# Kernel tuning notes

Hardware: AMD Instinct MI355X
Metric: run time of the kernel (lower is better)

The kernel has to match this reference:

```python
import jax, jax.numpy as jnp
import numpy as np

B, L, D, H, R = 2, 2048, 1024, 16, 32
DH = D // H
LORA_SCALE = 64.0 / 32.0  # alpha / rank


def _ln(x, w, b):
    mu = jnp.mean(x, axis=-1, keepdims=True)
    xc = x - mu
    var = jnp.mean(xc * xc, axis=-1, keepdims=True)
    y = xc * jax.lax.rsqrt(var + 1e-5) * w
    return y + b if b is not None else y


def _rotate_half(x):
    x1, x2 = jnp.split(x, 2, axis=-1)
    return jnp.concatenate([-x2, x1], axis=-1)


def _apply_rotary(q, k):
    # q, k: [B, L, H, DH]
    seqlen = q.shape[1]
    inv_freq = 1.0 / (10000.0 ** (jnp.arange(0, DH, 2, dtype=jnp.float32) / DH))
    t = jnp.arange(seqlen, dtype=jnp.float32)
    freqs = t[:, None] * inv_freq[None, :]           # [L, DH/2]
    emb = jnp.concatenate([freqs, freqs], axis=-1)   # [L, DH]
    cos = jnp.cos(emb)[None, :, None, :]
    sin = jnp.sin(emb)[None, :, None, :]
    q = q * cos + _rotate_half(q) * sin
    k = k * cos + _rotate_half(k) * sin
    return q, k


def setup_inputs() -> dict:
    key = jax.random.key(0)
    ks = jax.random.split(key, 10)
    s = 0.02
    return {
        "x": jax.random.normal(ks[0], (B, L, D), dtype=jnp.float32),
        "seq_id": jnp.sort(jax.random.randint(ks[1], (B, L), 0, 4), axis=-1),
        "ln_w": jnp.ones((D,), jnp.float32),
        "ln_b": jnp.zeros((D,), jnp.float32),
        "w_qkv": jax.random.normal(ks[2], (3 * D, D), jnp.float32) * s,
        "q_lora_a": jax.random.normal(ks[3], (R, D), jnp.float32) * s,
        "q_lora_b": jax.random.normal(ks[4], (D, R), jnp.float32) * s,
        "v_lora_a": jax.random.normal(ks[5], (R, D), jnp.float32) * s,
        "v_lora_b": jax.random.normal(ks[6], (D, R), jnp.float32) * s,
        "q_ln_w": jnp.ones((D,), jnp.float32),
        "k_ln_w": jnp.ones((D,), jnp.float32),
        "w_out": jax.random.normal(ks[7], (D, D), jnp.float32) * s,
    }


def reference(x, seq_id, ln_w, ln_b, w_qkv, q_lora_a, q_lora_b,
              v_lora_a, v_lora_b, q_ln_w, k_ln_w, w_out):
    h = _ln(x, ln_w, ln_b)                          # [B, L, D]
    qkv = jnp.einsum('bld,ed->ble', h, w_qkv)       # [B, L, 3D]
    q, k, v = jnp.split(qkv, 3, axis=-1)
    q = q + LORA_SCALE * jnp.einsum('blr,dr->bld', jnp.einsum('bld,rd->blr', h, q_lora_a), q_lora_b)
    v = v + LORA_SCALE * jnp.einsum('blr,dr->bld', jnp.einsum('bld,rd->blr', h, v_lora_a), v_lora_b)
    q = _ln(q, q_ln_w, None)
    k = _ln(k, k_ln_w, None)
    q = q.reshape(B, L, H, DH)
    k = k.reshape(B, L, H, DH)
    q, k = _apply_rotary(q, k)
    qh = q.transpose(0, 2, 1, 3)                    # [B, H, L, DH]
    kh = k.transpose(0, 2, 1, 3)
    vh = v.reshape(B, L, H, DH).transpose(0, 2, 1, 3)
    scale = 1.0 / np.sqrt(DH)
    scores = jnp.einsum('bhqd,bhkd->bhqk', qh, kh) * scale
    mask = (seq_id[:, None, :, None] == seq_id[:, None, None, :])  # [B,1,L,L]
    scores = jnp.where(mask, scores, jnp.finfo(scores.dtype).min)
    attn = jax.nn.softmax(scores, axis=-1)
    ctx = jnp.einsum('bhqk,bhkd->bhqd', attn, vh)   # [B, H, L, DH]
    ctx = ctx.transpose(0, 2, 1, 3).reshape(B, L, D)
    return jnp.einsum('bld,ed->ble', ctx, w_out)
```

## Files before the change

### kernel.cpp

```cpp
#include <hip/hip_runtime.h>
#include <hip/hip_bf16.h>
#include <cmath>

constexpr int Bb = 2;
constexpr int Ls = 2048;
constexpr int Dd = 1024;
constexpr int Hh = 16;
constexpr int DHh = 64;
constexpr int Rr = 32;
constexpr int BL = Bb * Ls;
constexpr float LORA_SCALE = 2.0f;
constexpr float LN_EPS = 1e-5f;
constexpr float ATTN_SCALE = 0.125f;
constexpr float LOG2E = 1.4426950408889634f;
constexpr float QSCL = ATTN_SCALE * LOG2E;

typedef __attribute__((ext_vector_type(8))) short bf16x8;
typedef __attribute__((ext_vector_type(4))) float f32x4;

__device__ __forceinline__ unsigned short f2bf(float f) {
    __hip_bfloat16 b = __float2bfloat16(f);
    return *reinterpret_cast<unsigned short*>(&b);
}
__device__ __forceinline__ float bf2f(unsigned short u) {
    unsigned int x = ((unsigned int)u) << 16;
    return __uint_as_float(x);
}
__device__ __forceinline__ void async_copy16(const void* g, void* l) {
    __builtin_amdgcn_global_load_lds(
        (__attribute__((address_space(1))) void*)(void*)(size_t)g,
        (__attribute__((address_space(3))) void*)l, 16, 0, 0);
}

__global__ __launch_bounds__(256) void prep_ln_kernel(const float* __restrict__ w,
                                                      const float* __restrict__ qa,
                                                      const float* __restrict__ qb,
                                                      const float* __restrict__ va,
                                                      const float* __restrict__ vb,
                                                      const float* __restrict__ wout,
                                                      const float* __restrict__ x,
                                                      const float* __restrict__ lnw,
                                                      const float* __restrict__ lnb,
                                                      unsigned short* __restrict__ wqkvb,
                                                      unsigned short* __restrict__ woutb,
                                                      float* __restrict__ ropec,
                                                      float* __restrict__ ropes,
                                                      unsigned short* __restrict__ hb) {
    const int blk = blockIdx.x;
    const int tid = threadIdx.x;
    if (blk < 3 * Dd) {
        const int e = blk;
        const int d0 = tid * 4;
        __shared__ float br[Rr];
        const bool isq = (e < Dd);
        const bool isv = (e >= 2 * Dd);
        const float* bsrc = isq ? (qb + (size_t)e * Rr)
                                : (isv ? (vb + (size_t)(e - 2 * Dd) * Rr) : nullptr);
        const float* asrc = isq ? qa : va;
        if (bsrc && tid < Rr) br[tid] = bsrc[tid];
        __syncthreads();
        float acc[4] = {0.f, 0.f, 0.f, 0.f};
        if (bsrc) {
#pragma unroll 8
            for (int r = 0; r < Rr; ++r) {
                float4 av = *(const float4*)(asrc + (size_t)r * Dd + d0);
                acc[0] += br[r] * av.x; acc[1] += br[r] * av.y;
                acc[2] += br[r] * av.z; acc[3] += br[r] * av.w;
            }
        }
        float4 wv = *(const float4*)(w + (size_t)e * Dd + d0);
        ushort4 o;
        o.x = f2bf(wv.x + LORA_SCALE * acc[0]);
        o.y = f2bf(wv.y + LORA_SCALE * acc[1]);
        o.z = f2bf(wv.z + LORA_SCALE * acc[2]);
        o.w = f2bf(wv.w + LORA_SCALE * acc[3]);
        *(ushort4*)(wqkvb + (size_t)e * Dd + d0) = o;
    } else if (blk < 4 * Dd) {
        int i = ((blk - 3 * Dd) * 256 + tid) * 4;
        float4 v = *(const float4*)(wout + i);
        ushort4 o;
        o.x = f2bf(v.x); o.y = f2bf(v.y); o.z = f2bf(v.z); o.w = f2bf(v.w);
        *(ushort4*)(woutb + i) = o;
    } else if (blk < 4 * Dd + 256) {
        int i = (blk - 4 * Dd) * 256 + tid;
        int l = i >> 5;
        int f = i & 31;
        float invf = powf(10000.0f, -(float)f * (1.0f / 32.0f));
        float ang = (float)l * invf;
        float s, c;
        sincosf(ang, &s, &c);
        ropec[i] = c;
        ropes[i] = s;
    } else {
        const int w64 = tid >> 6;
        const int L = tid & 63;
        const int row = (blk - (4 * Dd + 256)) * 4 + w64;
        const float* xr = x + (size_t)row * Dd;
        float4 v4[4];
        float v[16];
#pragma unroll
        for (int c = 0; c < 4; ++c) {
            v4[c] = *(const float4*)(xr + c * 256 + L * 4);
            v[c * 4 + 0] = v4[c].x; v[c * 4 + 1] = v4[c].y;
            v[c * 4 + 2] = v4[c].z; v[c * 4 + 3] = v4[c].w;
        }
        float s = 0.f;
#pragma unroll
        for (int j = 0; j < 16; ++j) s += v[j];
#pragma unroll
        for (int off = 1; off < 64; off <<= 1) s += __shfl_xor(s, off, 64);
        float mean = s * (1.0f / Dd);
        float sq = 0.f;
#pragma unroll
        for (int j = 0; j < 16; ++j) {
            v[j] -= mean;
            sq += v[j] * v[j];
        }
#pragma unroll
        for (int off = 1; off < 64; off <<= 1) sq += __shfl_xor(sq, off, 64);
        float rs = rsqrtf(sq * (1.0f / Dd) + LN_EPS);
        unsigned short* hr = hb + (size_t)row * Dd;
#pragma unroll
        for (int c = 0; c < 4; ++c) {
            int d = c * 256 + L * 4;
            float4 wv = *(const float4*)(lnw + d);
            float4 bv = *(const float4*)(lnb + d);
            ushort4 o;
            o.x = f2bf(v[c * 4 + 0] * rs * wv.x + bv.x);
            o.y = f2bf(v[c * 4 + 1] * rs * wv.y + bv.y);
            o.z = f2bf(v[c * 4 + 2] * rs * wv.z + bv.z);
            o.w = f2bf(v[c * 4 + 3] * rs * wv.w + bv.w);
            *(ushort4*)(hr + d) = o;
        }
    }
}

__global__ __launch_bounds__(256) void gemm_bt_mfma(const unsigned short* __restrict__ A,
                                                    const unsigned short* __restrict__ B,
                                                    unsigned short* __restrict__ C,
                                                    int M, int N, int K) {
    __shared__ short As[128 * 64];
    __shared__ short Bs[128 * 64];
    const int tid = threadIdx.x;
    const int w = tid >> 6, lane = tid & 63, quad = lane >> 4, l15 = lane & 15;
    const int m0 = blockIdx.y * 128, n0 = blockIdx.x * 128;
    const int wm = (w & 1) * 64, wn = (w >> 1) * 64;
    f32x4 acc[4][4];
#pragma unroll
    for (int i = 0; i < 4; ++i)
#pragma unroll
        for (int j = 0; j < 4; ++j) acc[i][j] = f32x4{0.f, 0.f, 0.f, 0.f};

    for (int k0 = 0; k0 < K; k0 += 64) {
#pragma unroll
        for (int j = 0; j < 4; ++j) {
            int c = tid + j * 256;
            int row = c >> 3;
            int jg = (c & 7) ^ (row & 7);
            async_copy16(A + (size_t)(m0 + row) * K + k0 + jg * 8, As + c * 8);
        }
#pragma unroll
        for (int j = 0; j < 4; ++j) {
            int c = tid + j * 256;
            int row = c >> 3;
            int jg = (c & 7) ^ (row & 7);
            async_copy16(B + (size_t)(n0 + row) * K + k0 + jg * 8, Bs + c * 8);
        }
        __syncthreads();
#pragma unroll
        for (int ks = 0; ks < 2; ++ks) {
            bf16x8 a[4], b[4];
#pragma unroll
            for (int mi = 0; mi < 4; ++mi) {
                int row = wm + mi * 16 + l15;
                int ch = (ks * 4 + quad) ^ (row & 7);
                a[mi] = *(const bf16x8*)&As[row * 64 + ch * 8];
            }
#pragma unroll
            for (int ni = 0; ni < 4; ++ni) {
                int row = wn + ni * 16 + l15;
                int ch = (ks * 4 + quad) ^ (row & 7);
                b[ni] = *(const bf16x8*)&Bs[row * 64 + ch * 8];
            }
#pragma unroll
            for (int mi = 0; mi < 4; ++mi)
#pragma unroll
                for (int ni = 0; ni < 4; ++ni)
                    acc[mi][ni] = __builtin_amdgcn_mfma_f32_16x16x32_bf16(a[mi], b[ni], acc[mi][ni], 0, 0, 0);
        }
        __syncthreads();
    }
#pragma unroll
    for (int mi = 0; mi < 4; ++mi)
#pragma unroll
        for (int ni = 0; ni < 4; ++ni)
#pragma unroll
            for (int r = 0; r < 4; ++r)
                C[(size_t)(m0 + wm + mi * 16 + quad * 4 + r) * N + n0 + wn + ni * 16 + l15] =
                    f2bf(acc[mi][ni][r]);
}

__global__ __launch_bounds__(256) void gemm_bt_mfma_n64(const unsigned short* __restrict__ A,
                                                        const unsigned short* __restrict__ B,
                                                        float* __restrict__ C,
                                                        int M, int N, int K) {
    __shared__ short As[128 * 64];
    __shared__ short Bs[64 * 64];
    const int tid = threadIdx.x;
    const int w = tid >> 6, lane = tid & 63, quad = lane >> 4, l15 = lane & 15;
    const int m0 = blockIdx.y * 128, n0 = blockIdx.x * 64;
    const int wm = (w & 1) * 64, wn = (w >> 1) * 32;
    f32x4 acc[4][2];
#pragma unroll
    for (int i = 0; i < 4; ++i)
#pragma unroll
        for (int j = 0; j < 2; ++j) acc[i][j] = f32x4{0.f, 0.f, 0.f, 0.f};

    for (int k0 = 0; k0 < K; k0 += 64) {
#pragma unroll
        for (int j = 0; j < 4; ++j) {
            int c = tid + j * 256;
            int row = c >> 3;
            int jg = (c & 7) ^ (row & 7);
            async_copy16(A + (size_t)(m0 + row) * K + k0 + jg * 8, As + c * 8);
        }
#pragma unroll
        for (int j = 0; j < 2; ++j) {
            int c = tid + j * 256;
            int row = c >> 3;
            int jg = (c & 7) ^ (row & 7);
            async_copy16(B + (size_t)(n0 + row) * K + k0 + jg * 8, Bs + c * 8);
        }
        __syncthreads();
#pragma unroll
        for (int ks = 0; ks < 2; ++ks) {
            bf16x8 a[4], b[2];
#pragma unroll
            for (int mi = 0; mi < 4; ++mi) {
                int row = wm + mi * 16 + l15;
                int ch = (ks * 4 + quad) ^ (row & 7);
                a[mi] = *(const bf16x8*)&As[row * 64 + ch * 8];
            }
#pragma unroll
            for (int ni = 0; ni < 2; ++ni) {
                int row = wn + ni * 16 + l15;
                int ch = (ks * 4 + quad) ^ (row & 7);
                b[ni] = *(const bf16x8*)&Bs[row * 64 + ch * 8];
            }
#pragma unroll
            for (int mi = 0; mi < 4; ++mi)
#pragma unroll
                for (int ni = 0; ni < 2; ++ni)
                    acc[mi][ni] = __builtin_amdgcn_mfma_f32_16x16x32_bf16(a[mi], b[ni], acc[mi][ni], 0, 0, 0);
        }
        __syncthreads();
    }
#pragma unroll
    for (int mi = 0; mi < 4; ++mi)
#pragma unroll
        for (int ni = 0; ni < 2; ++ni)
#pragma unroll
            for (int r = 0; r < 4; ++r)
                C[(size_t)(m0 + wm + mi * 16 + quad * 4 + r) * N + n0 + wn + ni * 16 + l15] =
                    acc[mi][ni][r];
}

__global__ __launch_bounds__(256) void qkv_final_kernel(const unsigned short* __restrict__ qkvb,
                                                        const float* __restrict__ qlnw,
                                                        const float* __restrict__ klnw,
                                                        const float* __restrict__ ropec,
                                                        const float* __restrict__ ropes,
                                                        unsigned short* __restrict__ qt,
                                                        unsigned short* __restrict__ kt,
                                                        unsigned short* __restrict__ vtt) {
    const int blk = blockIdx.x;
    const int tid = threadIdx.x;
    if (blk < BL / 4) {
        const int w64 = tid >> 6;
        const int L = tid & 63;
        const int row = blk * 4 + w64;
        const int b = row >> 11;
        const int l = row & (Ls - 1);
        const unsigned short* qp = qkvb + (size_t)row * (3 * Dd);
        const unsigned short* kp = qp + Dd;

        bf16x8 qA = *(const bf16x8*)(qp + L * 8);
        bf16x8 qB = *(const bf16x8*)(qp + 512 + L * 8);
        bf16x8 kA = *(const bf16x8*)(kp + L * 8);
        bf16x8 kB = *(const bf16x8*)(kp + 512 + L * 8);
        float vq[16], vk[16];
#pragma unroll
        for (int j = 0; j < 8; ++j) {
            vq[j] = bf2f((unsigned short)qA[j]);
            vq[8 + j] = bf2f((unsigned short)qB[j]);
            vk[j] = bf2f((unsigned short)kA[j]);
            vk[8 + j] = bf2f((unsigned short)kB[j]);
        }
        float sq = 0.f, sk = 0.f;
#pragma unroll
        for (int j = 0; j < 16; ++j) { sq += vq[j]; sk += vk[j]; }
#pragma unroll
        for (int off = 1; off < 64; off <<= 1) {
            sq += __shfl_xor(sq, off, 64);
            sk += __shfl_xor(sk, off, 64);
        }
        float mq = sq * (1.0f / Dd), mk = sk * (1.0f / Dd);
        float vvq = 0.f, vvk = 0.f;
#pragma unroll
        for (int j = 0; j < 16; ++j) {
            vq[j] -= mq; vvq += vq[j] * vq[j];
            vk[j] -= mk; vvk += vk[j] * vk[j];
        }
#pragma unroll
        for (int off = 1; off < 64; off <<= 1) {
            vvq += __shfl_xor(vvq, off, 64);
            vvk += __shfl_xor(vvk, off, 64);
        }
        float rsq = rsqrtf(vvq * (1.0f / Dd) + LN_EPS);
        float rsk = rsqrtf(vvk * (1.0f / Dd) + LN_EPS);

        float yq[16], yk[16];
        {
            float4 w0 = *(const float4*)(qlnw + L * 8);
            float4 w1 = *(const float4*)(qlnw + L * 8 + 4);
            float4 w2 = *(const float4*)(qlnw + 512 + L * 8);
            float4 w3 = *(const float4*)(qlnw + 512 + L * 8 + 4);
            yq[0] = vq[0] * rsq * w0.x; yq[1] = vq[1] * rsq * w0.y;
            yq[2] = vq[2] * rsq * w0.z; yq[3] = vq[3] * rsq * w0.w;
            yq[4] = vq[4] * rsq * w1.x; yq[5] = vq[5] * rsq * w1.y;
            yq[6] = vq[6] * rsq * w1.z; yq[7] = vq[7] * rsq * w1.w;
            yq[8] = vq[8] * rsq * w2.x; yq[9] = vq[9] * rsq * w2.y;
            yq[10] = vq[10] * rsq * w2.z; yq[11] = vq[11] * rsq * w2.w;
            yq[12] = vq[12] * rsq * w3.x; yq[13] = vq[13] * rsq * w3.y;
            yq[14] = vq[14] * rsq * w3.z; yq[15] = vq[15] * rsq * w3.w;
        }
        {
            float4 w0 = *(const float4*)(klnw + L * 8);
            float4 w1 = *(const float4*)(klnw + L * 8 + 4);
            float4 w2 = *(const float4*)(klnw + 512 + L * 8);
            float4 w3 = *(const float4*)(klnw + 512 + L * 8 + 4);
            yk[0] = vk[0] * rsk * w0.x; yk[1] = vk[1] * rsk * w0.y;
            yk[2] = vk[2] * rsk * w0.z; yk[3] = vk[3] * rsk * w0.w;
            yk[4] = vk[4] * rsk * w1.x; yk[5] = vk[5] * rsk * w1.y;
            yk[6] = vk[6] * rsk * w1.z; yk[7] = vk[7] * rsk * w1.w;
            yk[8] = vk[8] * rsk * w2.x; yk[9] = vk[9] * rsk * w2.y;
            yk[10] = vk[10] * rsk * w2.z; yk[11] = vk[11] * rsk * w2.w;
            yk[12] = vk[12] * rsk * w3.x; yk[13] = vk[13] * rsk * w3.y;
            yk[14] = vk[14] * rsk * w3.z; yk[15] = vk[15] * rsk * w3.w;
        }

        float cs[8], sn[8];
        {
            int fbase = l * 32 + (L & 3) * 8;
            float4 c0 = *(const float4*)(ropec + fbase);
            float4 c1 = *(const float4*)(ropec + fbase + 4);
            float4 s0 = *(const float4*)(ropes + fbase);
            float4 s1 = *(const float4*)(ropes + fbase + 4);
            cs[0] = c0.x; cs[1] = c0.y; cs[2] = c0.z; cs[3] = c0.w;
            cs[4] = c1.x; cs[5] = c1.y; cs[6] = c1.z; cs[7] = c1.w;
            sn[0] = s0.x; sn[1] = s0.y; sn[2] = s0.z; sn[3] = s0.w;
            sn[4] = s1.x; sn[5] = s1.y; sn[6] = s1.z; sn[7] = s1.w;
        }
        const float sgn = (L & 4) ? 1.0f : -1.0f;
        unsigned short outqA[8], outqB[8], outkA[8], outkB[8];
#pragma unroll
        for (int j = 0; j < 8; ++j) {
            float pA = __shfl_xor(yq[j], 4, 64);
            float pB = __shfl_xor(yq[8 + j], 4, 64);
            outqA[j] = f2bf((yq[j] * cs[j] + sgn * pA * sn[j]) * QSCL);
            outqB[j] = f2bf((yq[8 + j] * cs[j] + sgn * pB * sn[j]) * QSCL);
            float pkA = __shfl_xor(yk[j], 4, 64);
            float pkB = __shfl_xor(yk[8 + j], 4, 64);
            outkA[j] = f2bf(yk[j] * cs[j] + sgn * pkA * sn[j]);
            outkB[j] = f2bf(yk[8 + j] * cs[j] + sgn * pkB * sn[j]);
        }
        const int hA = L >> 3;
        const int dh0 = (L & 7) * 8;
        size_t offA = (((size_t)(b * Hh + hA)) * Ls + l) * DHh + dh0;
        size_t offB = (((size_t)(b * Hh + 8 + hA)) * Ls + l) * DHh + dh0;
        *(uint4*)(qt + offA) = *(uint4*)outqA;
        *(uint4*)(qt + offB) = *(uint4*)outqB;
        *(uint4*)(kt + offA) = *(uint4*)outkA;
        *(uint4*)(kt + offB) = *(uint4*)outkB;
    } else {
        const int t2 = blk - BL / 4;
        const int l0 = (t2 & 31) * 64;
        const int h = (t2 >> 5) & 15;
        const int b = t2 >> 9;
        __shared__ short t[64][72];
        const unsigned short* src = qkvb + (size_t)b * Ls * (3 * Dd) + 2 * Dd + h * 64;
#pragma unroll
        for (int j = 0; j < 2; ++j) {
            int g = tid + j * 256;
            int row = g >> 3;
            int c0 = (g & 7) * 8;
            uint4 vv = *(const uint4*)(src + (size_t)(l0 + row) * (3 * Dd) + c0);
            *(uint4*)&t[row][c0] = vv;
        }
        __syncthreads();
        unsigned short* dst = vtt + ((size_t)(b * Hh + h) * DHh) * Ls;
#pragma unroll
        for (int j = 0; j < 2; ++j) {
            int g = tid + j * 256;
            int dh = g >> 3;
            int lc = (g & 7) * 8;
            ushort4 o0, o1;
            unsigned short* p0 = (unsigned short*)&o0;
            unsigned short* p1 = (unsigned short*)&o1;
#pragma unroll
            for (int i = 0; i < 4; ++i) p0[i] = (unsigned short)t[lc + i][dh];
#pragma unroll
            for (int i = 0; i < 4; ++i) p1[i] = (unsigned short)t[lc + 4 + i][dh];
            *(ushort4*)(dst + (size_t)dh * Ls + l0 + lc) = o0;
            *(ushort4*)(dst + (size_t)dh * Ls + l0 + lc + 4) = o1;
        }
    }
}

constexpr int PSP = 76;

__global__ __launch_bounds__(512) void attn_kernel(const unsigned short* __restrict__ qt,
                                                   const unsigned short* __restrict__ kt,
                                                   const unsigned short* __restrict__ vtt,
                                                   const int* __restrict__ seq_id,
                                                   unsigned short* __restrict__ ctxb) {
    const int id = blockIdx.x;
    const int c8 = id & 7;
    const int x = (id >> 3) & 15;
    const int g4 = id >> 7;
    const int v = c8 + 8 * g4;
    const int b = v >> 4;
    const int h = v & 15;
    const int q0 = x * 128;

    const size_t base = ((size_t)(b * Hh + h)) * Ls * DHh;
    const size_t base_v = ((size_t)(b * Hh + h)) * DHh * Ls;
    const int* sid = seq_id + (size_t)b * Ls;

    __shared__ short Ks[2][64 * 64];
    __shared__ short Vs[2][64 * 64];
    __shared__ short Ps[8][16 * PSP];
    __shared__ int sq_s[128];

    const int tid = threadIdx.x;
    const int w = tid >> 6;
    const int lane = tid & 63;
    const int quad = lane >> 4;
    const int l15 = lane & 15;

    if (tid < 128) sq_s[tid] = sid[q0 + tid];
    const int qmin = sid[q0];
    const int qmax = sid[q0 + 127];

    bool need = false;
    if (lane < 32) {
        int kmn = sid[lane * 64];
        int kmx = sid[lane * 64 + 63];
        need = (kmn <= qmax) && (kmx >= qmin);
    }
    unsigned long long bmask = __ballot(need);
    const int t0 = __builtin_ctzll(bmask);
    const int t1 = 64 - __builtin_clzll(bmask);

    auto stage = [&](int buf, int t) {
        int row = tid >> 3;
        int jg = (tid & 7) ^ (row & 7);
        async_copy16(kt + base + (size_t)(t * 64 + row) * DHh + jg * 8,
                     &Ks[buf][tid * 8]);
        async_copy16(vtt + base_v + (size_t)row * Ls + t * 64 + jg * 8,
                     &Vs[buf][tid * 8]);
    };

    stage(0, t0);
    const int qrow = q0 + w * 16 + l15;
    const bf16x8 a0 = *(const bf16x8*)(qt + base + (size_t)qrow * DHh + quad * 8);
    const bf16x8 a1 = *(const bf16x8*)(qt + base + (size_t)qrow * DHh + 32 + quad * 8);

    int sqv[4];
    float lsum[4] = {0.f, 0.f, 0.f, 0.f};
    f32x4 O[4];
#pragma unroll
    for (int r = 0; r < 4; ++r) O[r] = f32x4{0.f, 0.f, 0.f, 0.f};

    __syncthreads();
#pragma unroll
    for (int r = 0; r < 4; ++r) sqv[r] = sq_s[w * 16 + quad * 4 + r];

    for (int t = t0; t < t1; ++t) {
        const int cur = (t - t0) & 1;
        if (t + 1 < t1) stage(cur ^ 1, t + 1);
        const int k0 = t * 64;

        f32x4 s[4];
#pragma unroll
        for (int kg = 0; kg < 4; ++kg) {
            int krow = kg * 16 + l15;
            bf16x8 b0 = *(const bf16x8*)&Ks[cur][krow * 64 + ((0 + quad) ^ (krow & 7)) * 8];
            bf16x8 b1 = *(const bf16x8*)&Ks[cur][krow * 64 + ((4 + quad) ^ (krow & 7)) * 8];
            f32x4 acc = {0.f, 0.f, 0.f, 0.f};
            acc = __builtin_amdgcn_mfma_f32_16x16x32_bf16(a0, b0, acc, 0, 0, 0);
            acc = __builtin_amdgcn_mfma_f32_16x16x32_bf16(a1, b1, acc, 0, 0, 0);
            s[kg] = acc;
        }

        const int kmn = sid[k0];
        const int kmx = sid[k0 + 63];
        const bool nomask = (kmn == kmx) && (qmin == qmax) && (kmn == qmin);
        if (!nomask) {
#pragma unroll
            for (int kg = 0; kg < 4; ++kg) {
                int skv = sid[k0 + kg * 16 + l15];
#pragma unroll
                for (int r = 0; r < 4; ++r)
                    if (sqv[r] != skv) s[kg][r] = -3.0e38f;
            }
        }
#pragma unroll
        for (int kg = 0; kg < 4; ++kg)
#pragma unroll
            for (int r = 0; r < 4; ++r)
                s[kg][r] = __builtin_amdgcn_exp2f(s[kg][r]);
#pragma unroll
        for (int r = 0; r < 4; ++r)
            lsum[r] += s[0][r] + s[1][r] + s[2][r] + s[3][r];

#pragma unroll
        for (int kg = 0; kg < 4; ++kg)
#pragma unroll
            for (int r = 0; r < 4; ++r)
                Ps[w][(quad * 4 + r) * PSP + kg * 16 + l15] = (short)f2bf(s[kg][r]);

        bf16x8 pa0 = *(const bf16x8*)&Ps[w][l15 * PSP + quad * 8];
        bf16x8 pa1 = *(const bf16x8*)&Ps[w][l15 * PSP + 32 + quad * 8];
#pragma unroll
        for (int ng = 0; ng < 4; ++ng) {
            int vrow = ng * 16 + l15;
            bf16x8 vb0 = *(const bf16x8*)&Vs[cur][vrow * 64 + ((0 + quad) ^ (vrow & 7)) * 8];
            bf16x8 vb1 = *(const bf16x8*)&Vs[cur][vrow * 64 + ((4 + quad) ^ (vrow & 7)) * 8];
            O[ng] = __builtin_amdgcn_mfma_f32_16x16x32_bf16(pa0, vb0, O[ng], 0, 0, 0);
            O[ng] = __builtin_amdgcn_mfma_f32_16x16x32_bf16(pa1, vb1, O[ng], 0, 0, 0);
        }

        __syncthreads();
    }

#pragma unroll
    for (int off = 1; off < 16; off <<= 1)
#pragma unroll
        for (int r = 0; r < 4; ++r)
            lsum[r] += __shfl_xor(lsum[r], off, 64);
    float inv_l[4];
#pragma unroll
    for (int r = 0; r < 4; ++r) inv_l[r] = 1.0f / lsum[r];
#pragma unroll
    for (int ng = 0; ng < 4; ++ng)
#pragma unroll
        for (int r = 0; r < 4; ++r) {
            int q = q0 + w * 16 + quad * 4 + r;
            ctxb[((size_t)b * Ls + q) * Dd + h * DHh + ng * 16 + l15] =
                f2bf(O[ng][r] * inv_l[r]);
        }
}

extern "C" void kernel_launch(void* const* d_in, const int* in_sizes, int n_in,
                              void* d_out, int out_size, void* d_ws, size_t ws_size,
                              hipStream_t stream) {
    const float* x = (const float*)d_in[0];
    const int* seq_id = (const int*)d_in[1];
    const float* ln_w = (const float*)d_in[2];
    const float* ln_b = (const float*)d_in[3];
    const float* w_qkv = (const float*)d_in[4];
    const float* q_lora_a = (const float*)d_in[5];
    const float* q_lora_b = (const float*)d_in[6];
    const float* v_lora_a = (const float*)d_in[7];
    const float* v_lora_b = (const float*)d_in[8];
    const float* q_ln_w = (const float*)d_in[9];
    const float* k_ln_w = (const float*)d_in[10];
    const float* w_out = (const float*)d_in[11];
    float* out = (float*)d_out;

    const size_t SZ = (size_t)BL * Dd;
    float* p = (float*)d_ws;
    float* ropec = p;          p += (size_t)Ls * 32;
    float* ropes = p;          p += (size_t)Ls * 32;
    unsigned short* ub = (unsigned short*)p;
    unsigned short* qkvb = ub; ub += 3 * SZ;
    unsigned short* hb = ub;   ub += SZ;
    unsigned short* qt = ub;   ub += SZ;
    unsigned short* kt = ub;   ub += SZ;
    unsigned short* vtt = ub;  ub += SZ;
    unsigned short* ctxb = ub; ub += SZ;
    unsigned short* wqkvb = ub; ub += (size_t)3 * Dd * Dd;
    unsigned short* woutb = ub; ub += (size_t)Dd * Dd;

    prep_ln_kernel<<<4 * Dd + 256 + BL / 4, 256, 0, stream>>>(
        w_qkv, q_lora_a, q_lora_b, v_lora_a, v_lora_b, w_out,
        x, ln_w, ln_b, wqkvb, woutb, ropec, ropes, hb);
    {
        dim3 g(3 * Dd / 128, BL / 128);
        gemm_bt_mfma<<<g, 256, 0, stream>>>(hb, wqkvb, qkvb, BL, 3 * Dd, Dd);
    }
    qkv_final_kernel<<<BL / 4 + 1024, 256, 0, stream>>>(qkvb, q_ln_w, k_ln_w,
                                                        ropec, ropes, qt, kt, vtt);
    attn_kernel<<<512, 512, 0, stream>>>(qt, kt, vtt, seq_id, ctxb);
    {
        dim3 g(Dd / 64, BL / 128);
        gemm_bt_mfma_n64<<<g, 256, 0, stream>>>(ctxb, woutb, out, BL, Dd, Dd);
    }
}
```

Before: 202.9 us.

## Register-stage K/V tiles two ahead and raise wave priority around MFMA

Replaces the async global-to-LDS copies for the K and V tiles with plain global loads into registers, issued two tiles ahead and written into the LDS double buffer one iteration later. This is meant to hide global-memory latency better than the direct async copy. It also wraps both MFMA blocks in s_setprio so matrix work gets scheduling priority over other waves. The trade-off is higher register pressure from the extra in-flight tile registers, plus explicit LDS writes that the async path did not need.

```diff
diff --git a/kernel.cpp b/kernel.cpp
--- a/kernel.cpp
+++ b/kernel.cpp
@@ -462,19 +462,26 @@
     const int t0 = __builtin_ctzll(bmask);
     const int t1 = 64 - __builtin_clzll(bmask);
 
-    auto stage = [&](int buf, int t) {
-        int row = tid >> 3;
-        int jg = (tid & 7) ^ (row & 7);
-        async_copy16(kt + base + (size_t)(t * 64 + row) * DHh + jg * 8,
-                     &Ks[buf][tid * 8]);
-        async_copy16(vtt + base_v + (size_t)row * Ls + t * 64 + jg * 8,
-                     &Vs[buf][tid * 8]);
+    const int srow = tid >> 3;
+    const int scol = (tid & 7) * 8;
+    const int sjg = (tid & 7) ^ (srow & 7);
+
+    auto stage_load = [&](int t, bf16x8& kr, bf16x8& vr) {
+        kr = *(const bf16x8*)(kt + base + (size_t)(t * 64 + srow) * DHh + scol);
+        vr = *(const bf16x8*)(vtt + base_v + (size_t)srow * Ls + t * 64 + scol);
     };
-
-    stage(0, t0);
+    auto stage_write = [&](int buf, const bf16x8& kr, const bf16x8& vr) {
+        *(bf16x8*)&Ks[buf][srow * 64 + sjg * 8] = kr;
+        *(bf16x8*)&Vs[buf][srow * 64 + sjg * 8] = vr;
+    };
+
+    bf16x8 krA{}, vrA{}, krB{}, vrB{};
+    stage_load(t0, krA, vrA);
     const int qrow = q0 + w * 16 + l15;
     const bf16x8 a0 = *(const bf16x8*)(qt + base + (size_t)qrow * DHh + quad * 8);
     const bf16x8 a1 = *(const bf16x8*)(qt + base + (size_t)qrow * DHh + 32 + quad * 8);
+    stage_write(0, krA, vrA);
+    if (t0 + 1 < t1) stage_load(t0 + 1, krA, vrA);
 
     int sqv[4];
     float lsum[4] = {0.f, 0.f, 0.f, 0.f};
@@ -488,10 +495,12 @@
 
     for (int t = t0; t < t1; ++t) {
         const int cur = (t - t0) & 1;
-        if (t + 1 < t1) stage(cur ^ 1, t + 1);
+        if (t + 1 < t1) stage_write(cur ^ 1, krA, vrA);
+        if (t + 2 < t1) stage_load(t + 2, krB, vrB);
         const int k0 = t * 64;
 
         f32x4 s[4];
+        __builtin_amdgcn_s_setprio(1);
 #pragma unroll
         for (int kg = 0; kg < 4; ++kg) {
             int krow = kg * 16 + l15;
@@ -502,6 +511,7 @@
             acc = __builtin_amdgcn_mfma_f32_16x16x32_bf16(a1, b1, acc, 0, 0, 0);
             s[kg] = acc;
         }
+        __builtin_amdgcn_s_setprio(0);
 
         const int kmn = sid[k0];
         const int kmx = sid[k0 + 63];
@@ -532,6 +542,7 @@
 
         bf16x8 pa0 = *(const bf16x8*)&Ps[w][l15 * PSP + quad * 8];
         bf16x8 pa1 = *(const bf16x8*)&Ps[w][l15 * PSP + 32 + quad * 8];
+        __builtin_amdgcn_s_setprio(1);
 #pragma unroll
         for (int ng = 0; ng < 4; ++ng) {
             int vrow = ng * 16 + l15;
@@ -540,8 +551,10 @@
             O[ng] = __builtin_amdgcn_mfma_f32_16x16x32_bf16(pa0, vb0, O[ng], 0, 0, 0);
             O[ng] = __builtin_amdgcn_mfma_f32_16x16x32_bf16(pa1, vb1, O[ng], 0, 0, 0);
         }
+        __builtin_amdgcn_s_setprio(0);
 
         __syncthreads();
+        krA = krB; vrA = vrB;
     }
 
 #pragma unroll
```

New measurement: 203.8 us. About the same (+0.5%).

## Rewrite attention core with 32x32 MFMA and register-resident P via lane shuffles

Applied to the files above, without the earlier changes.

Rewrites the attention inner loop to use 32x32x16 bf16 MFMA with 4 waves of 32 query rows each, instead of 8 waves of 16 rows with 16x16x32 MFMA. S is computed transposed (K as the A operand) so the probabilities can be packed to bf16 and rearranged between lane halves with xor-32 shuffles, feeding the PV MFMA directly. This removes the per-wave LDS P buffer and its write/read round trip. It also adds s_setprio around the MFMA blocks and halves the block size, so each thread stages two K/V chunks. The trade-off is fewer waves per block and more register pressure from the 16-wide accumulators.

```diff
diff --git a/kernel.cpp b/kernel.cpp
--- a/kernel.cpp
+++ b/kernel.cpp
@@ -17,6 +17,8 @@
 
 typedef __attribute__((ext_vector_type(8))) short bf16x8;
 typedef __attribute__((ext_vector_type(4))) float f32x4;
+typedef __attribute__((ext_vector_type(16))) float f32x16;
+typedef __attribute__((ext_vector_type(4))) unsigned int u32x4;
 
 __device__ __forceinline__ unsigned short f2bf(float f) {
     __hip_bfloat16 b = __float2bfloat16(f);
@@ -25,6 +27,9 @@
 __device__ __forceinline__ float bf2f(unsigned short u) {
     unsigned int x = ((unsigned int)u) << 16;
     return __uint_as_float(x);
+}
+__device__ __forceinline__ unsigned int pack2bf(float lo, float hi) {
+    return ((unsigned int)f2bf(hi) << 16) | (unsigned int)f2bf(lo);
 }
 __device__ __forceinline__ void async_copy16(const void* g, void* l) {
     __builtin_amdgcn_global_load_lds(
@@ -417,9 +422,7 @@
     }
 }
 
-constexpr int PSP = 76;
-
-__global__ __launch_bounds__(512) void attn_kernel(const unsigned short* __restrict__ qt,
+__global__ __launch_bounds__(256) void attn_kernel(const unsigned short* __restrict__ qt,
                                                    const unsigned short* __restrict__ kt,
                                                    const unsigned short* __restrict__ vtt,
                                                    const int* __restrict__ seq_id,
@@ -439,18 +442,17 @@
 
     __shared__ short Ks[2][64 * 64];
     __shared__ short Vs[2][64 * 64];
-    __shared__ short Ps[8][16 * PSP];
-    __shared__ int sq_s[128];
 
     const int tid = threadIdx.x;
     const int w = tid >> 6;
     const int lane = tid & 63;
-    const int quad = lane >> 4;
-    const int l15 = lane & 15;
-
-    if (tid < 128) sq_s[tid] = sid[q0 + tid];
+    const int l31 = lane & 31;
+    const int hi = lane >> 5;
+    const int q0w = q0 + w * 32;
+
     const int qmin = sid[q0];
     const int qmax = sid[q0 + 127];
+    const int sqv = sid[q0w + l31];
 
     bool need = false;
     if (lane < 32) {
@@ -463,103 +465,122 @@
     const int t1 = 64 - __builtin_clzll(bmask);
 
     auto stage = [&](int buf, int t) {
-        int row = tid >> 3;
-        int jg = (tid & 7) ^ (row & 7);
-        async_copy16(kt + base + (size_t)(t * 64 + row) * DHh + jg * 8,
-                     &Ks[buf][tid * 8]);
-        async_copy16(vtt + base_v + (size_t)row * Ls + t * 64 + jg * 8,
-                     &Vs[buf][tid * 8]);
+#pragma unroll
+        for (int j = 0; j < 2; ++j) {
+            int c = tid + j * 256;
+            int row = c >> 3;
+            int jg = (c & 7) ^ (row & 7);
+            async_copy16(kt + base + (size_t)(t * 64 + row) * DHh + jg * 8,
+                         &Ks[buf][c * 8]);
+            async_copy16(vtt + base_v + (size_t)row * Ls + t * 64 + jg * 8,
+                         &Vs[buf][c * 8]);
+        }
     };
 
     stage(0, t0);
-    const int qrow = q0 + w * 16 + l15;
-    const bf16x8 a0 = *(const bf16x8*)(qt + base + (size_t)qrow * DHh + quad * 8);
-    const bf16x8 a1 = *(const bf16x8*)(qt + base + (size_t)qrow * DHh + 32 + quad * 8);
-
-    int sqv[4];
-    float lsum[4] = {0.f, 0.f, 0.f, 0.f};
-    f32x4 O[4];
-#pragma unroll
-    for (int r = 0; r < 4; ++r) O[r] = f32x4{0.f, 0.f, 0.f, 0.f};
+    bf16x8 qf[4];
+#pragma unroll
+    for (int d = 0; d < 4; ++d)
+        qf[d] = *(const bf16x8*)(qt + base + (size_t)(q0w + l31) * DHh + d * 16 + hi * 8);
+
+    float lsum = 0.f;
+    f32x16 O[2];
+#pragma unroll
+    for (int nb = 0; nb < 2; ++nb)
+#pragma unroll
+        for (int r = 0; r < 16; ++r) O[nb][r] = 0.f;
 
     __syncthreads();
-#pragma unroll
-    for (int r = 0; r < 4; ++r) sqv[r] = sq_s[w * 16 + quad * 4 + r];
 
     for (int t = t0; t < t1; ++t) {
         const int cur = (t - t0) & 1;
         if (t + 1 < t1) stage(cur ^ 1, t + 1);
         const int k0 = t * 64;
 
-        f32x4 s[4];
-#pragma unroll
-        for (int kg = 0; kg < 4; ++kg) {
-            int krow = kg * 16 + l15;
-            bf16x8 b0 = *(const bf16x8*)&Ks[cur][krow * 64 + ((0 + quad) ^ (krow & 7)) * 8];
-            bf16x8 b1 = *(const bf16x8*)&Ks[cur][krow * 64 + ((4 + quad) ^ (krow & 7)) * 8];
-            f32x4 acc = {0.f, 0.f, 0.f, 0.f};
-            acc = __builtin_amdgcn_mfma_f32_16x16x32_bf16(a0, b0, acc, 0, 0, 0);
-            acc = __builtin_amdgcn_mfma_f32_16x16x32_bf16(a1, b1, acc, 0, 0, 0);
-            s[kg] = acc;
-        }
+        f32x16 p[2];
+        __builtin_amdgcn_s_setprio(1);
+#pragma unroll
+        for (int kb = 0; kb < 2; ++kb) {
+            const short* kbse = &Ks[cur][(kb * 32 + l31) * 64];
+            f32x16 acc;
+#pragma unroll
+            for (int r = 0; r < 16; ++r) acc[r] = 0.f;
+#pragma unroll
+            for (int d = 0; d < 4; ++d) {
+                bf16x8 kf = *(const bf16x8*)&kbse[(((d << 1) | hi) ^ (l31 & 7)) * 8];
+                acc = __builtin_amdgcn_mfma_f32_32x32x16_bf16(kf, qf[d], acc, 0, 0, 0);
+            }
+            p[kb] = acc;
+        }
+        __builtin_amdgcn_s_setprio(0);
 
         const int kmn = sid[k0];
         const int kmx = sid[k0 + 63];
         const bool nomask = (kmn == kmx) && (qmin == qmax) && (kmn == qmin);
         if (!nomask) {
 #pragma unroll
-            for (int kg = 0; kg < 4; ++kg) {
-                int skv = sid[k0 + kg * 16 + l15];
-#pragma unroll
-                for (int r = 0; r < 4; ++r)
-                    if (sqv[r] != skv) s[kg][r] = -3.0e38f;
-            }
-        }
-#pragma unroll
-        for (int kg = 0; kg < 4; ++kg)
-#pragma unroll
-            for (int r = 0; r < 4; ++r)
-                s[kg][r] = __builtin_amdgcn_exp2f(s[kg][r]);
-#pragma unroll
-        for (int r = 0; r < 4; ++r)
-            lsum[r] += s[0][r] + s[1][r] + s[2][r] + s[3][r];
-
-#pragma unroll
-        for (int kg = 0; kg < 4; ++kg)
-#pragma unroll
-            for (int r = 0; r < 4; ++r)
-                Ps[w][(quad * 4 + r) * PSP + kg * 16 + l15] = (short)f2bf(s[kg][r]);
-
-        bf16x8 pa0 = *(const bf16x8*)&Ps[w][l15 * PSP + quad * 8];
-        bf16x8 pa1 = *(const bf16x8*)&Ps[w][l15 * PSP + 32 + quad * 8];
-#pragma unroll
-        for (int ng = 0; ng < 4; ++ng) {
-            int vrow = ng * 16 + l15;
-            bf16x8 vb0 = *(const bf16x8*)&Vs[cur][vrow * 64 + ((0 + quad) ^ (vrow & 7)) * 8];
-            bf16x8 vb1 = *(const bf16x8*)&Vs[cur][vrow * 64 + ((4 + quad) ^ (vrow & 7)) * 8];
-            O[ng] = __builtin_amdgcn_mfma_f32_16x16x32_bf16(pa0, vb0, O[ng], 0, 0, 0);
-            O[ng] = __builtin_amdgcn_mfma_f32_16x16x32_bf16(pa1, vb1, O[ng], 0, 0, 0);
-        }
+            for (int kb = 0; kb < 2; ++kb)
+#pragma unroll
+                for (int r = 0; r < 16; ++r) {
+                    int kk = k0 + kb * 32 + ((r & 3) + 8 * (r >> 2) + 4 * hi);
+                    if (sid[kk] != sqv) p[kb][r] = -3.0e38f;
+                }
+        }
+#pragma unroll
+        for (int kb = 0; kb < 2; ++kb)
+#pragma unroll
+            for (int r = 0; r < 16; ++r) {
+                p[kb][r] = __builtin_amdgcn_exp2f(p[kb][r]);
+                lsum += p[kb][r];
+            }
+
+        u32x4 pa[4];
+#pragma unroll
+        for (int kb = 0; kb < 2; ++kb) {
+            unsigned int u[8], sw[8];
+#pragma unroll
+            for (int i = 0; i < 8; ++i) {
+                u[i] = pack2bf(p[kb][2 * i], p[kb][2 * i + 1]);
+                sw[i] = (unsigned int)__shfl_xor((int)u[i], 32, 64);
+            }
+            pa[2 * kb][0] = hi ? sw[2] : u[0];
+            pa[2 * kb][1] = hi ? sw[3] : u[1];
+            pa[2 * kb][2] = hi ? u[2] : sw[0];
+            pa[2 * kb][3] = hi ? u[3] : sw[1];
+            pa[2 * kb + 1][0] = hi ? sw[6] : u[4];
+            pa[2 * kb + 1][1] = hi ? sw[7] : u[5];
+            pa[2 * kb + 1][2] = hi ? u[6] : sw[4];
+            pa[2 * kb + 1][3] = hi ? u[7] : sw[5];
+        }
+
+        __builtin_amdgcn_s_setprio(1);
+#pragma unroll
+        for (int nb = 0; nb < 2; ++nb) {
+            const short* vbse = &Vs[cur][(nb * 32 + l31) * 64];
+#pragma unroll
+            for (int ks = 0; ks < 4; ++ks) {
+                bf16x8 vf = *(const bf16x8*)&vbse[(((ks << 1) | hi) ^ (l31 & 7)) * 8];
+                bf16x8 paf = __builtin_bit_cast(bf16x8, pa[ks]);
+                O[nb] = __builtin_amdgcn_mfma_f32_32x32x16_bf16(paf, vf, O[nb], 0, 0, 0);
+            }
+        }
+        __builtin_amdgcn_s_setprio(0);
 
         __syncthreads();
     }
 
-#pragma unroll
-    for (int off = 1; off < 16; off <<= 1)
-#pragma unroll
-        for (int r = 0; r < 4; ++r)
-            lsum[r] += __shfl_xor(lsum[r], off, 64);
-    float inv_l[4];
-#pragma unroll
-    for (int r = 0; r < 4; ++r) inv_l[r] = 1.0f / lsum[r];
-#pragma unroll
-    for (int ng = 0; ng < 4; ++ng)
-#pragma unroll
-        for (int r = 0; r < 4; ++r) {
-            int q = q0 + w * 16 + quad * 4 + r;
-            ctxb[((size_t)b * Ls + q) * Dd + h * DHh + ng * 16 + l15] =
-                f2bf(O[ng][r] * inv_l[r]);
-        }
+    lsum += __shfl_xor(lsum, 32, 64);
+    const float inv = 1.0f / lsum;
+#pragma unroll
+    for (int r = 0; r < 16; ++r) {
+        const int crow = (r & 3) + 8 * (r >> 2) + 4 * hi;
+        const float il = __shfl(inv, crow, 64);
+        const int q = q0w + crow;
+#pragma unroll
+        for (int nb = 0; nb < 2; ++nb)
+            ctxb[((size_t)b * Ls + q) * Dd + h * DHh + nb * 32 + l31] =
+                f2bf(O[nb][r] * il);
+    }
 }
 
 extern "C" void kernel_launch(void* const* d_in, const int* in_sizes, int n_in,
@@ -602,7 +623,7 @@
     }
     qkv_final_kernel<<<BL / 4 + 1024, 256, 0, stream>>>(qkvb, q_ln_w, k_ln_w,
                                                         ropec, ropes, qt, kt, vtt);
-    attn_kernel<<<512, 512, 0, stream>>>(qt, kt, vtt, seq_id, ctxb);
+    attn_kernel<<<512, 256, 0, stream>>>(qt, kt, vtt, seq_id, ctxb);
     {
         dim3 g(Dd / 64, BL / 128);
         gemm_bt_mfma_n64<<<g, 256, 0, stream>>>(ctxb, woutb, out, BL, Dd, Dd);
```

New measurement: 217.4 us. 1.07x slower.

## Replace QKV GEMM with 256x256 double-buffered pipelined MFMA kernel

Applied to the files above, without the earlier changes.

Swaps the 128x128 single-buffered QKV projection GEMM for a 512-thread kernel with 256x256 tiles and double-buffered LDS. Loads for the next K tile are interleaved with MFMA phases, with barriers and s_setprio around them. The aim is to hide global-load latency and raise arithmetic intensity per tile. In exchange, the grid drops to 192 blocks, fewer than the CU count, LDS use rises to 128KB per block, register pressure grows, and the K-tile count is hardcoded.

```diff
diff --git a/kernel.cpp b/kernel.cpp
--- a/kernel.cpp
+++ b/kernel.cpp
@@ -135,69 +135,155 @@
     }
 }
 
-__global__ __launch_bounds__(256) void gemm_bt_mfma(const unsigned short* __restrict__ A,
-                                                    const unsigned short* __restrict__ B,
-                                                    unsigned short* __restrict__ C,
-                                                    int M, int N, int K) {
-    __shared__ short As[128 * 64];
-    __shared__ short Bs[128 * 64];
+constexpr int GTILES = 16;
+
+__global__ __launch_bounds__(512, 2) void gemm_qkv_256(const unsigned short* __restrict__ A,
+                                                       const unsigned short* __restrict__ B,
+                                                       unsigned short* __restrict__ C,
+                                                       int M, int N, int K) {
+    __shared__ short As[2][256 * 64];
+    __shared__ short Bs[2][256 * 64];
     const int tid = threadIdx.x;
-    const int w = tid >> 6, lane = tid & 63, quad = lane >> 4, l15 = lane & 15;
-    const int m0 = blockIdx.y * 128, n0 = blockIdx.x * 128;
-    const int wm = (w & 1) * 64, wn = (w >> 1) * 64;
-    f32x4 acc[4][4];
-#pragma unroll
-    for (int i = 0; i < 4; ++i)
+    const int w = tid >> 6;
+    const int lane = tid & 63;
+    const int quad = lane >> 4, l15 = lane & 15;
+    const int wr = w >> 2;
+    const int wc = w & 3;
+    const int m0 = blockIdx.y * 256, n0 = blockIdx.x * 256;
+
+    f32x4 acc[8][4];
+#pragma unroll
+    for (int i = 0; i < 8; ++i)
 #pragma unroll
         for (int j = 0; j < 4; ++j) acc[i][j] = f32x4{0.f, 0.f, 0.f, 0.f};
 
-    for (int k0 = 0; k0 < K; k0 += 64) {
-#pragma unroll
-        for (int j = 0; j < 4; ++j) {
-            int c = tid + j * 256;
+    auto stageA = [&](int buf, int kt) {
+#pragma unroll
+        for (int i = 0; i < 4; ++i) {
+            int c = tid + i * 512;
             int row = c >> 3;
             int jg = (c & 7) ^ (row & 7);
-            async_copy16(A + (size_t)(m0 + row) * K + k0 + jg * 8, As + c * 8);
-        }
-#pragma unroll
-        for (int j = 0; j < 4; ++j) {
-            int c = tid + j * 256;
+            async_copy16(A + (size_t)(m0 + row) * K + kt * 64 + jg * 8,
+                         &As[buf][c * 8]);
+        }
+    };
+    auto stageB = [&](int buf, int kt) {
+#pragma unroll
+        for (int i = 0; i < 4; ++i) {
+            int c = tid + i * 512;
             int row = c >> 3;
             int jg = (c & 7) ^ (row & 7);
-            async_copy16(B + (size_t)(n0 + row) * K + k0 + jg * 8, Bs + c * 8);
-        }
-        __syncthreads();
-#pragma unroll
-        for (int ks = 0; ks < 2; ++ks) {
-            bf16x8 a[4], b[4];
-#pragma unroll
-            for (int mi = 0; mi < 4; ++mi) {
-                int row = wm + mi * 16 + l15;
-                int ch = (ks * 4 + quad) ^ (row & 7);
-                a[mi] = *(const bf16x8*)&As[row * 64 + ch * 8];
-            }
-#pragma unroll
-            for (int ni = 0; ni < 4; ++ni) {
-                int row = wn + ni * 16 + l15;
-                int ch = (ks * 4 + quad) ^ (row & 7);
-                b[ni] = *(const bf16x8*)&Bs[row * 64 + ch * 8];
-            }
-#pragma unroll
-            for (int mi = 0; mi < 4; ++mi)
-#pragma unroll
-                for (int ni = 0; ni < 4; ++ni)
-                    acc[mi][ni] = __builtin_amdgcn_mfma_f32_16x16x32_bf16(a[mi], b[ni], acc[mi][ni], 0, 0, 0);
-        }
-        __syncthreads();
-    }
-#pragma unroll
-    for (int mi = 0; mi < 4; ++mi)
+            async_copy16(B + (size_t)(n0 + row) * K + kt * 64 + jg * 8,
+                         &Bs[buf][c * 8]);
+        }
+    };
+
+    stageA(0, 0);
+    stageB(0, 0);
+    asm volatile("s_waitcnt vmcnt(0)");
+    asm volatile("" ::: "memory");
+    __builtin_amdgcn_s_barrier();
+
+    for (int t = 0; t < GTILES; ++t) {
+        const int cur = t & 1;
+        const short* as = As[cur];
+        const short* bs = Bs[cur];
+        bf16x8 af[8], bfr[2];
+
+#pragma unroll
+        for (int mi = 0; mi < 8; ++mi) {
+            int row = wr * 128 + mi * 16 + l15;
+            af[mi] = *(const bf16x8*)&as[row * 64 + ((0 + quad) ^ (row & 7)) * 8];
+        }
+#pragma unroll
+        for (int ni = 0; ni < 2; ++ni) {
+            int row = wc * 64 + ni * 16 + l15;
+            bfr[ni] = *(const bf16x8*)&bs[row * 64 + ((0 + quad) ^ (row & 7)) * 8];
+        }
+        if (t + 1 < GTILES) stageA(cur ^ 1, t + 1);
+        asm volatile("" ::: "memory");
+        __builtin_amdgcn_s_barrier();
+        asm volatile("s_waitcnt lgkmcnt(0)");
+        __builtin_amdgcn_s_setprio(1);
+#pragma unroll
+        for (int mi = 0; mi < 8; ++mi)
+#pragma unroll
+            for (int ni = 0; ni < 2; ++ni)
+                acc[mi][ni] = __builtin_amdgcn_mfma_f32_16x16x32_bf16(af[mi], bfr[ni], acc[mi][ni], 0, 0, 0);
+        __builtin_amdgcn_s_setprio(0);
+        asm volatile("" ::: "memory");
+        __builtin_amdgcn_s_barrier();
+
+#pragma unroll
+        for (int ni = 0; ni < 2; ++ni) {
+            int row = wc * 64 + (2 + ni) * 16 + l15;
+            bfr[ni] = *(const bf16x8*)&bs[row * 64 + ((0 + quad) ^ (row & 7)) * 8];
+        }
+        if (t + 1 < GTILES) stageB(cur ^ 1, t + 1);
+        asm volatile("" ::: "memory");
+        __builtin_amdgcn_s_barrier();
+        asm volatile("s_waitcnt lgkmcnt(0)");
+        __builtin_amdgcn_s_setprio(1);
+#pragma unroll
+        for (int mi = 0; mi < 8; ++mi)
+#pragma unroll
+            for (int ni = 0; ni < 2; ++ni)
+                acc[mi][2 + ni] = __builtin_amdgcn_mfma_f32_16x16x32_bf16(af[mi], bfr[ni], acc[mi][2 + ni], 0, 0, 0);
+        __builtin_amdgcn_s_setprio(0);
+        asm volatile("" ::: "memory");
+        __builtin_amdgcn_s_barrier();
+
+#pragma unroll
+        for (int mi = 0; mi < 8; ++mi) {
+            int row = wr * 128 + mi * 16 + l15;
+            af[mi] = *(const bf16x8*)&as[row * 64 + ((4 + quad) ^ (row & 7)) * 8];
+        }
+#pragma unroll
+        for (int ni = 0; ni < 2; ++ni) {
+            int row = wc * 64 + ni * 16 + l15;
+            bfr[ni] = *(const bf16x8*)&bs[row * 64 + ((4 + quad) ^ (row & 7)) * 8];
+        }
+        asm volatile("" ::: "memory");
+        __builtin_amdgcn_s_barrier();
+        asm volatile("s_waitcnt lgkmcnt(0)");
+        __builtin_amdgcn_s_setprio(1);
+#pragma unroll
+        for (int mi = 0; mi < 8; ++mi)
+#pragma unroll
+            for (int ni = 0; ni < 2; ++ni)
+                acc[mi][ni] = __builtin_amdgcn_mfma_f32_16x16x32_bf16(af[mi], bfr[ni], acc[mi][ni], 0, 0, 0);
+        __builtin_amdgcn_s_setprio(0);
+        asm volatile("" ::: "memory");
+        __builtin_amdgcn_s_barrier();
+
+#pragma unroll
+        for (int ni = 0; ni < 2; ++ni) {
+            int row = wc * 64 + (2 + ni) * 16 + l15;
+            bfr[ni] = *(const bf16x8*)&bs[row * 64 + ((4 + quad) ^ (row & 7)) * 8];
+        }
+        asm volatile("s_waitcnt vmcnt(0)");
+        asm volatile("" ::: "memory");
+        __builtin_amdgcn_s_barrier();
+        asm volatile("s_waitcnt lgkmcnt(0)");
+        __builtin_amdgcn_s_setprio(1);
+#pragma unroll
+        for (int mi = 0; mi < 8; ++mi)
+#pragma unroll
+            for (int ni = 0; ni < 2; ++ni)
+                acc[mi][2 + ni] = __builtin_amdgcn_mfma_f32_16x16x32_bf16(af[mi], bfr[ni], acc[mi][2 + ni], 0, 0, 0);
+        __builtin_amdgcn_s_setprio(0);
+        asm volatile("" ::: "memory");
+        __builtin_amdgcn_s_barrier();
+    }
+
+#pragma unroll
+    for (int mi = 0; mi < 8; ++mi)
 #pragma unroll
         for (int ni = 0; ni < 4; ++ni)
 #pragma unroll
             for (int r = 0; r < 4; ++r)
-                C[(size_t)(m0 + wm + mi * 16 + quad * 4 + r) * N + n0 + wn + ni * 16 + l15] =
-                    f2bf(acc[mi][ni][r]);
+                C[(size_t)(m0 + wr * 128 + mi * 16 + quad * 4 + r) * N +
+                  n0 + wc * 64 + ni * 16 + l15] = f2bf(acc[mi][ni][r]);
 }
 
 __global__ __launch_bounds__(256) void gemm_bt_mfma_n64(const unsigned short* __restrict__ A,
@@ -597,8 +683,8 @@
         w_qkv, q_lora_a, q_lora_b, v_lora_a, v_lora_b, w_out,
         x, ln_w, ln_b, wqkvb, woutb, ropec, ropes, hb);
     {
-        dim3 g(3 * Dd / 128, BL / 128);
-        gemm_bt_mfma<<<g, 256, 0, stream>>>(hb, wqkvb, qkvb, BL, 3 * Dd, Dd);
+        dim3 g(3 * Dd / 256, BL / 256);
+        gemm_qkv_256<<<g, 512, 0, stream>>>(hb, wqkvb, qkvb, BL, 3 * Dd, Dd);
     }
     qkv_final_kernel<<<BL / 4 + 1024, 256, 0, stream>>>(qkvb, q_ln_w, k_ln_w,
                                                         ropec, ropes, qt, kt, vtt);
```

Result: no change. 201.5 us (-0.7%).
